# Kernel tuning notes

Hardware: AMD Instinct MI355X
Metric: run time of the kernel (lower is better)

## Reference

```python
import jax, jax.numpy as jnp
import numpy as np

NUM_HEADS = 4


def setup_inputs() -> dict:
    key = jax.random.key(0)
    k1, k2, k3 = jax.random.split(key, 3)
    B, NN, C = 1, 256, 128
    x = jax.random.normal(k1, (B, NN, C), dtype=jnp.float32)
    # Linear(d_model, 4*d_model, bias=False); stored as (in, out) for x @ W_w
    W_w = jax.random.normal(k2, (C, 4 * C), dtype=jnp.float32) * (C ** -0.5)
    # proj = Linear(d_model, d_model) with bias; stored as (in, out)
    W_proj = jax.random.normal(k3, (C, C), dtype=jnp.float32) * (C ** -0.5)
    b_proj = jnp.zeros((C,), dtype=jnp.float32)
    return {"x": x, "W_w": W_w, "W_proj": W_proj, "b_proj": b_proj}


def reference(x, W_w, W_proj, b_proj):
    B, NN, C = x.shape
    H = NUM_HEADS
    D = C // H
    scale = D ** -0.5
    # qkv-style projection: (B, NN, 4, H, D) -> (4, B, H, NN, D)
    w = (x @ W_w).reshape(B, NN, 4, H, D).transpose(2, 0, 3, 1, 4)
    a, b, c, v = w[0], w[1], w[2], w[3]
    AB = jnp.einsum('bhid,bhjd->bhij', a, b) * scale
    CD = jnp.einsum('bhid,bhkd->bhik', a, c) * scale
    EF = jnp.einsum('bhjd,bhkd->bhjk', b, c) * scale
    # Triplet scores: (B, H, NN, NN, NN)
    A_ijk = AB[..., :, :, None] + CD[..., :, None, :] + EF[..., None, :, :]
    e = jnp.exp(A_ijk)
    # Normalize over (i, j) for each k, per original sum(dim=(-2,-3))
    norm = jnp.clip(e.sum(axis=(-2, -3), keepdims=True), 1e-6, None)
    en = e / norm
    x1 = jnp.einsum('bhijk,bhjd->bhid', en, v)
    x2 = jnp.einsum('bhijk,bhkd->bhid', en, v)
    out = (x1 * x2).transpose(0, 2, 1, 3).reshape(B, NN, C)
    return out @ W_proj + b_proj
```

## Files before the change

kernel.cpp:

```cpp
#include <hip/hip_runtime.h>
#include <hip/hip_bf16.h>


constexpr size_t OFF_W     = 0;
constexpr size_t OFF_P     = 131072;
constexpr size_t OFF_Q     = OFF_P + 262144;
constexpr size_t OFF_RT    = OFF_Q + 262144;
constexpr size_t OFF_T     = OFF_RT + 262144;
constexpr size_t OFF_NORMP = OFF_T + 524288;

__global__ __launch_bounds__(256) void k_w(const float* __restrict__ x,
                                           const float* __restrict__ Ww,
                                           float* __restrict__ w,
                                           const float* __restrict__ bp,
                                           float* __restrict__ out) {
    __shared__ __align__(16) float As[1152];
    __shared__ __align__(16) float Bs[1152];
    int j0 = blockIdx.x * 32, i0 = blockIdx.y * 32;
    int t = threadIdx.x, tx = t & 15, ty = t >> 4, r = t >> 3, g = t & 7;
    {
        int oidx = (blockIdx.y * 16 + blockIdx.x) * 256 + t;
        out[oidx] = bp[oidx & 127];
    }
    float4 a4 = *(const float4*)&x[(size_t)(i0 + r) * 128 + g * 4];
    float4 b4 = *(const float4*)&Ww[(size_t)r * 512 + j0 + g * 4];
    float a00 = 0, a01 = 0, a10 = 0, a11 = 0;
    for (int kc = 0; kc < 128; kc += 32) {
        As[(g * 4 + 0) * 36 + r] = a4.x; As[(g * 4 + 1) * 36 + r] = a4.y;
        As[(g * 4 + 2) * 36 + r] = a4.z; As[(g * 4 + 3) * 36 + r] = a4.w;
        *(float4*)&Bs[r * 36 + g * 4] = b4;
        __syncthreads();
        if (kc + 32 < 128) {
            a4 = *(const float4*)&x[(size_t)(i0 + r) * 128 + kc + 32 + g * 4];
            b4 = *(const float4*)&Ww[(size_t)(kc + 32 + r) * 512 + j0 + g * 4];
        }
#pragma unroll
        for (int kk = 0; kk < 32; kk++) {
            float2 av = *(float2*)&As[kk * 36 + ty * 2];
            float2 bv = *(float2*)&Bs[kk * 36 + tx * 2];
            a00 += av.x * bv.x; a01 += av.x * bv.y;
            a10 += av.y * bv.x; a11 += av.y * bv.y;
        }
        __syncthreads();
    }
    *(float2*)&w[(size_t)(i0 + ty * 2) * 512 + j0 + tx * 2] = make_float2(a00, a01);
    *(float2*)&w[(size_t)(i0 + ty * 2 + 1) * 512 + j0 + tx * 2] = make_float2(a10, a11);
}

__global__ __launch_bounds__(256, 2) void k_T(const float* __restrict__ w,
                                              float* __restrict__ P,
                                              float* __restrict__ Q,
                                              float* __restrict__ Rt,
                                              float* __restrict__ T,
                                              float* __restrict__ normp) {
    __shared__ __align__(16) float aT[1152];
    __shared__ __align__(16) float cT[1152];
    __shared__ __align__(16) float bT[1152];
    __shared__ __align__(16) float PsT[1152];
    __shared__ __align__(16) float RsT[1152];
    int h = blockIdx.z >> 1, jh = blockIdx.z & 1;
    int k0 = blockIdx.x * 32, i0 = blockIdx.y * 32;
    int jc0 = jh * 128;
    size_t hb = (size_t)h * 65536;
    int t = threadIdx.x, tx = t & 15, ty = t >> 4, r = t >> 3, g = t & 7;
    const float sc = 0.17677669529663687f;

    float4 av = *(const float4*)&w[(size_t)(i0 + r) * 512 + h * 32 + g * 4];
    aT[(g * 4 + 0) * 36 + r] = av.x; aT[(g * 4 + 1) * 36 + r] = av.y;
    aT[(g * 4 + 2) * 36 + r] = av.z; aT[(g * 4 + 3) * 36 + r] = av.w;
    float4 cv = *(const float4*)&w[(size_t)(k0 + r) * 512 + 256 + h * 32 + g * 4];
    cT[(g * 4 + 0) * 36 + r] = cv.x; cT[(g * 4 + 1) * 36 + r] = cv.y;
    cT[(g * 4 + 2) * 36 + r] = cv.z; cT[(g * 4 + 3) * 36 + r] = cv.w;
    float4 bv = *(const float4*)&w[(size_t)(jc0 + r) * 512 + 128 + h * 32 + g * 4];
    __syncthreads();

    float2 a_tx[32], c_tx[32];
#pragma unroll
    for (int d = 0; d < 32; d++) {
        a_tx[d] = *(float2*)&aT[d * 36 + 2 * tx];
        c_tx[d] = *(float2*)&cT[d * 36 + 2 * tx];
    }

    float dq00 = 0, dq01 = 0, dq10 = 0, dq11 = 0;
#pragma unroll
    for (int d = 0; d < 32; d++) {
        float2 a2 = *(float2*)&aT[d * 36 + 2 * ty];
        float2 c2 = c_tx[d];
        dq00 += a2.x * c2.x; dq01 += a2.x * c2.y;
        dq10 += a2.y * c2.x; dq11 += a2.y * c2.y;
    }
    float q00 = __expf(sc * dq00), q01 = __expf(sc * dq01);
    float q10 = __expf(sc * dq10), q11 = __expf(sc * dq11);
    if (jh == 0) {
        *(float2*)&Q[hb + (size_t)(i0 + ty * 2) * 256 + k0 + tx * 2] = make_float2(q00, q01);
        *(float2*)&Q[hb + (size_t)(i0 + ty * 2 + 1) * 256 + k0 + tx * 2] = make_float2(q10, q11);
    }

    const bool wP = (k0 == 0), wR = (blockIdx.y == 0);
    float acc00 = 0, acc01 = 0, acc10 = 0, acc11 = 0;
    for (int jc = jc0; jc < jc0 + 128; jc += 32) {
        bT[(g * 4 + 0) * 36 + r] = bv.x; bT[(g * 4 + 1) * 36 + r] = bv.y;
        bT[(g * 4 + 2) * 36 + r] = bv.z; bT[(g * 4 + 3) * 36 + r] = bv.w;
        __syncthreads();
        if (jc + 32 < jc0 + 128)
            bv = *(const float4*)&w[(size_t)(jc + 32 + r) * 512 + 128 + h * 32 + g * 4];
        float dp00 = 0, dp01 = 0, dp10 = 0, dp11 = 0;
        float dr00 = 0, dr01 = 0, dr10 = 0, dr11 = 0;
#pragma unroll
        for (int d = 0; d < 32; d++) {
            float2 b2 = *(float2*)&bT[d * 36 + 2 * ty];
            float2 a2 = a_tx[d];
            float2 c2 = c_tx[d];
            dp00 += b2.x * a2.x; dp01 += b2.x * a2.y;
            dp10 += b2.y * a2.x; dp11 += b2.y * a2.y;
            dr00 += b2.x * c2.x; dr01 += b2.x * c2.y;
            dr10 += b2.y * c2.x; dr11 += b2.y * c2.y;
        }
        float p00 = __expf(sc * dp00), p01 = __expf(sc * dp01);
        float p10 = __expf(sc * dp10), p11 = __expf(sc * dp11);
        float r00 = __expf(sc * dr00), r01 = __expf(sc * dr01);
        float r10 = __expf(sc * dr10), r11 = __expf(sc * dr11);
        *(float2*)&PsT[(2 * tx + 0) * 36 + 2 * ty] = make_float2(p00, p10);
        *(float2*)&PsT[(2 * tx + 1) * 36 + 2 * ty] = make_float2(p01, p11);
        *(float2*)&RsT[(2 * tx + 0) * 36 + 2 * ty] = make_float2(r00, r10);
        *(float2*)&RsT[(2 * tx + 1) * 36 + 2 * ty] = make_float2(r01, r11);
        if (wP) {
            *(float2*)&P[hb + (size_t)(i0 + tx * 2 + 0) * 256 + jc + ty * 2] = make_float2(p00, p10);
            *(float2*)&P[hb + (size_t)(i0 + tx * 2 + 1) * 256 + jc + ty * 2] = make_float2(p01, p11);
        }
        if (wR) {
            *(float2*)&Rt[hb + (size_t)(k0 + tx * 2 + 0) * 256 + jc + ty * 2] = make_float2(r00, r10);
            *(float2*)&Rt[hb + (size_t)(k0 + tx * 2 + 1) * 256 + jc + ty * 2] = make_float2(r01, r11);
        }
        __syncthreads();
#pragma unroll
        for (int q = 0; q < 8; q++) {
            float4 pA = *(float4*)&PsT[(2 * ty + 0) * 36 + 4 * q];
            float4 pB = *(float4*)&PsT[(2 * ty + 1) * 36 + 4 * q];
            float4 rA = *(float4*)&RsT[(2 * tx + 0) * 36 + 4 * q];
            float4 rB = *(float4*)&RsT[(2 * tx + 1) * 36 + 4 * q];
            acc00 += pA.x * rA.x + pA.y * rA.y + pA.z * rA.z + pA.w * rA.w;
            acc01 += pA.x * rB.x + pA.y * rB.y + pA.z * rB.z + pA.w * rB.w;
            acc10 += pB.x * rA.x + pB.y * rA.y + pB.z * rA.z + pB.w * rA.w;
            acc11 += pB.x * rB.x + pB.y * rB.y + pB.z * rB.z + pB.w * rB.w;
        }
    }
    float* Tp = T + (size_t)jh * 262144;
    *(float2*)&Tp[hb + (size_t)(i0 + ty * 2) * 256 + k0 + tx * 2] = make_float2(acc00, acc01);
    *(float2*)&Tp[hb + (size_t)(i0 + ty * 2 + 1) * 256 + k0 + tx * 2] = make_float2(acc10, acc11);
    __syncthreads();
    float* red = PsT;
    red[ty * 34 + tx * 2]     = q00 * acc00 + q10 * acc10;
    red[ty * 34 + tx * 2 + 1] = q01 * acc01 + q11 * acc11;
    __syncthreads();
    if (t < 32) {
        float s = 0.f;
#pragma unroll
        for (int m = 0; m < 16; m++) s += red[m * 34 + t];
        normp[h * 4096 + (jh * 8 + blockIdx.y) * 256 + k0 + t] = s;
    }
}

__global__ __launch_bounds__(256) void k_x1x2S(
    const float* __restrict__ P, const float* __restrict__ Q,
    const float* __restrict__ Rt, const float* __restrict__ T,
    const float* __restrict__ normp, const float* __restrict__ w,
    const float* __restrict__ Wp, float* __restrict__ out) {
    int h = blockIdx.y;
    int i0 = blockIdx.x * 4;
    size_t hb = (size_t)h * 65536;
    __shared__ float rn_s[256];
    __shared__ __align__(16) float qs[1024];
    __shared__ __align__(16) float Ss[1024];
    __shared__ __align__(16) float wp[1024];
    __shared__ __align__(16) float wq[1024];
    __shared__ __align__(16) float vT[8320];
    __shared__ float ys[144];
    int t = threadIdx.x;
    {
        float s = 0.f;
#pragma unroll
        for (int ib = 0; ib < 16; ib++) s += normp[h * 4096 + ib * 256 + t];
        rn_s[t] = 1.f / fmaxf(s, 1e-6f);
    }
    __syncthreads();
    {
        int row = t >> 6, jq = (t & 63) * 4;
        float4 q4 = *(const float4*)&Q[hb + (size_t)(i0 + row) * 256 + jq];
        float4 rn4 = *(float4*)&rn_s[jq];
        q4.x *= rn4.x; q4.y *= rn4.y; q4.z *= rn4.z; q4.w *= rn4.w;
        *(float4*)&qs[row * 256 + jq] = q4;
    }
    __syncthreads();
    {
        int jq = (t & 63) * 4, kq = t >> 6;
        float4 acc0 = {0, 0, 0, 0}, acc1 = {0, 0, 0, 0};
        float4 acc2 = {0, 0, 0, 0}, acc3 = {0, 0, 0, 0};
#pragma unroll 8
        for (int kk = 0; kk < 64; kk++) {
            int k = kq * 64 + kk;
            float4 r4 = *(const float4*)&Rt[hb + (size_t)k * 256 + jq];
            float q0 = qs[0 * 256 + k], q1 = qs[1 * 256 + k];
            float q2 = qs[2 * 256 + k], q3 = qs[3 * 256 + k];
            acc0.x += q0 * r4.x; acc0.y += q0 * r4.y; acc0.z += q0 * r4.z; acc0.w += q0 * r4.w;
            acc1.x += q1 * r4.x; acc1.y += q1 * r4.y; acc1.z += q1 * r4.z; acc1.w += q1 * r4.w;
            acc2.x += q2 * r4.x; acc2.y += q2 * r4.y; acc2.z += q2 * r4.z; acc2.w += q2 * r4.w;
            acc3.x += q3 * r4.x; acc3.y += q3 * r4.y; acc3.z += q3 * r4.z; acc3.w += q3 * r4.w;
        }
        float* red = vT;
        *(float4*)&red[(kq * 4 + 0) * 256 + jq] = acc0;
        *(float4*)&red[(kq * 4 + 1) * 256 + jq] = acc1;
        *(float4*)&red[(kq * 4 + 2) * 256 + jq] = acc2;
        *(float4*)&red[(kq * 4 + 3) * 256 + jq] = acc3;
    }
    __syncthreads();
    {
        int row = t >> 6, jq = (t & 63) * 4;
        float* red = vT;
        float4 s0 = *(float4*)&red[(0 * 4 + row) * 256 + jq];
        float4 s1 = *(float4*)&red[(1 * 4 + row) * 256 + jq];
        float4 s2 = *(float4*)&red[(2 * 4 + row) * 256 + jq];
        float4 s3 = *(float4*)&red[(3 * 4 + row) * 256 + jq];
        float4 sm;
        sm.x = (s0.x + s1.x) + (s2.x + s3.x);
        sm.y = (s0.y + s1.y) + (s2.y + s3.y);
        sm.z = (s0.z + s1.z) + (s2.z + s3.z);
        sm.w = (s0.w + s1.w) + (s2.w + s3.w);
        *(float4*)&Ss[row * 256 + jq] = sm;
    }
    __syncthreads();
#pragma unroll
    for (int m = 0; m < 8; m++) {
        int jj = m * 32 + (t >> 3);
        int dd = (t & 7) * 4;
        float4 v4 = *(const float4*)&w[(size_t)jj * 512 + 384 + h * 32 + dd];
        vT[(dd + 0) * 260 + jj] = v4.x;
        vT[(dd + 1) * 260 + jj] = v4.y;
        vT[(dd + 2) * 260 + jj] = v4.z;
        vT[(dd + 3) * 260 + jj] = v4.w;
    }
    {
        int rr = t >> 6, jj = (t & 63) * 4;
        size_t o = hb + (size_t)(i0 + rr) * 256 + jj;
        float4 p4  = *(const float4*)&P[o];
        float4 t4a = *(const float4*)&T[o];
        float4 t4b = *(const float4*)&T[o + 262144];
        float4 q4  = *(float4*)&qs[rr * 256 + jj];
        float4 s4  = *(float4*)&Ss[rr * 256 + jj];
        float4 wpv, wqv;
        wpv.x = p4.x * s4.x; wpv.y = p4.y * s4.y;
        wpv.z = p4.z * s4.z; wpv.w = p4.w * s4.w;
        wqv.x = q4.x * (t4a.x + t4b.x); wqv.y = q4.y * (t4a.y + t4b.y);
        wqv.z = q4.z * (t4a.z + t4b.z); wqv.w = q4.w * (t4a.w + t4b.w);
        *(float4*)&wp[rr * 256 + jj] = wpv;
        *(float4*)&wq[rr * 256 + jj] = wqv;
    }
    __syncthreads();
    int d = t & 31, rl = (t >> 5) & 3, jh2 = t >> 7;
    int jbase = jh2 * 128;
    float x1 = 0.f, x2 = 0.f;
#pragma unroll
    for (int q = 0; q < 32; q++) {
        int j = jbase + 4 * q;
        float4 wp4 = *(float4*)&wp[rl * 256 + j];
        float4 wq4 = *(float4*)&wq[rl * 256 + j];
        float4 v4  = *(float4*)&vT[d * 260 + j];
        x1 += wp4.x * v4.x + wp4.y * v4.y + wp4.z * v4.z + wp4.w * v4.w;
        x2 += wq4.x * v4.x + wq4.y * v4.y + wq4.z * v4.z + wq4.w * v4.w;
    }
    __syncthreads();
    float* redx = wp;
    float* redy = wq;
    redx[t] = x1;
    redy[t] = x2;
    float* Wps = vT;
#pragma unroll
    for (int m = 0; m < 4; m++) {
        int idx = m * 256 + t;
        int k = idx >> 5, n = (idx & 31) * 4;
        *(float4*)&Wps[k * 128 + n] = *(const float4*)&Wp[(size_t)(h * 32 + k) * 128 + n];
    }
    __syncthreads();
    if (t < 128) {
        float x1t = redx[t] + redx[t + 128];
        float x2t = redy[t] + redy[t + 128];
        ys[rl * 33 + d] = x1t * x2t;
    }
    __syncthreads();
    int n = t & 127, ti = t >> 7;
    float acc0 = 0.f, acc1 = 0.f;
#pragma unroll
    for (int k = 0; k < 32; k++) {
        float wv = Wps[k * 128 + n];
        acc0 += ys[(ti + 0) * 33 + k] * wv;
        acc1 += ys[(ti + 2) * 33 + k] * wv;
    }
    atomicAdd(&out[(size_t)(i0 + ti + 0) * 128 + n], acc0);
    atomicAdd(&out[(size_t)(i0 + ti + 2) * 128 + n], acc1);
}

extern "C" void kernel_launch(void* const* d_in, const int* in_sizes, int n_in,
                              void* d_out, int out_size, void* d_ws, size_t ws_size,
                              hipStream_t stream) {
    const float* x      = (const float*)d_in[0];
    const float* W_w    = (const float*)d_in[1];
    const float* W_proj = (const float*)d_in[2];
    const float* b_proj = (const float*)d_in[3];
    float* out = (float*)d_out;
    float* ws  = (float*)d_ws;

    float* w     = ws + OFF_W;
    float* P     = ws + OFF_P;
    float* Q     = ws + OFF_Q;
    float* Rt    = ws + OFF_RT;
    float* T     = ws + OFF_T;
    float* normp = ws + OFF_NORMP;

    k_w<<<dim3(16, 8), 256, 0, stream>>>(x, W_w, w, b_proj, out);
    k_T<<<dim3(8, 8, 8), 256, 0, stream>>>(w, P, Q, Rt, T, normp);
    k_x1x2S<<<dim3(64, 4), 256, 0, stream>>>(P, Q, Rt, T, normp, w, W_proj, out);
}
```

Before: 36.52 us.

## Split k_T j-range into four partial slices and pad LDS stride to 38

The j reduction in k_T is now split four ways instead of two, doubling the grid to 1024 blocks, each covering 64 j columns. Four partial T buffers and twice as many normp partials are written, and the consumer kernel sums all of them. The shared-memory row stride also changes from 36 to 38 to alter bank mapping. This is meant to give more parallelism and shorten each block's serial loop, at the cost of redundant a/c/Q setup per block and extra partial-sum traffic.

Result: slower. 41.75 us (+14.3%).

```diff
diff --git a/kernel.cpp b/kernel.cpp
--- a/kernel.cpp
+++ b/kernel.cpp
@@ -7,7 +7,7 @@
 constexpr size_t OFF_Q     = OFF_P + 262144;
 constexpr size_t OFF_RT    = OFF_Q + 262144;
 constexpr size_t OFF_T     = OFF_RT + 262144;
-constexpr size_t OFF_NORMP = OFF_T + 524288;
+constexpr size_t OFF_NORMP = OFF_T + 1048576;
 
 __global__ __launch_bounds__(256) void k_w(const float* __restrict__ x,
                                            const float* __restrict__ Ww,
@@ -53,62 +53,62 @@
                                               float* __restrict__ Rt,
                                               float* __restrict__ T,
                                               float* __restrict__ normp) {
-    __shared__ __align__(16) float aT[1152];
-    __shared__ __align__(16) float cT[1152];
-    __shared__ __align__(16) float bT[1152];
-    __shared__ __align__(16) float PsT[1152];
-    __shared__ __align__(16) float RsT[1152];
-    int h = blockIdx.z >> 1, jh = blockIdx.z & 1;
+    __shared__ __align__(16) float aT[1216];
+    __shared__ __align__(16) float cT[1216];
+    __shared__ __align__(16) float bT[1216];
+    __shared__ __align__(16) float PsT[1216];
+    __shared__ __align__(16) float RsT[1216];
+    int h = blockIdx.z >> 2, jq = blockIdx.z & 3;
     int k0 = blockIdx.x * 32, i0 = blockIdx.y * 32;
-    int jc0 = jh * 128;
+    int jc0 = jq * 64;
     size_t hb = (size_t)h * 65536;
     int t = threadIdx.x, tx = t & 15, ty = t >> 4, r = t >> 3, g = t & 7;
     const float sc = 0.17677669529663687f;
 
     float4 av = *(const float4*)&w[(size_t)(i0 + r) * 512 + h * 32 + g * 4];
-    aT[(g * 4 + 0) * 36 + r] = av.x; aT[(g * 4 + 1) * 36 + r] = av.y;
-    aT[(g * 4 + 2) * 36 + r] = av.z; aT[(g * 4 + 3) * 36 + r] = av.w;
+    aT[(g * 4 + 0) * 38 + r] = av.x; aT[(g * 4 + 1) * 38 + r] = av.y;
+    aT[(g * 4 + 2) * 38 + r] = av.z; aT[(g * 4 + 3) * 38 + r] = av.w;
     float4 cv = *(const float4*)&w[(size_t)(k0 + r) * 512 + 256 + h * 32 + g * 4];
-    cT[(g * 4 + 0) * 36 + r] = cv.x; cT[(g * 4 + 1) * 36 + r] = cv.y;
-    cT[(g * 4 + 2) * 36 + r] = cv.z; cT[(g * 4 + 3) * 36 + r] = cv.w;
+    cT[(g * 4 + 0) * 38 + r] = cv.x; cT[(g * 4 + 1) * 38 + r] = cv.y;
+    cT[(g * 4 + 2) * 38 + r] = cv.z; cT[(g * 4 + 3) * 38 + r] = cv.w;
     float4 bv = *(const float4*)&w[(size_t)(jc0 + r) * 512 + 128 + h * 32 + g * 4];
     __syncthreads();
 
     float2 a_tx[32], c_tx[32];
 #pragma unroll
     for (int d = 0; d < 32; d++) {
-        a_tx[d] = *(float2*)&aT[d * 36 + 2 * tx];
-        c_tx[d] = *(float2*)&cT[d * 36 + 2 * tx];
+        a_tx[d] = *(float2*)&aT[d * 38 + 2 * tx];
+        c_tx[d] = *(float2*)&cT[d * 38 + 2 * tx];
     }
 
     float dq00 = 0, dq01 = 0, dq10 = 0, dq11 = 0;
 #pragma unroll
     for (int d = 0; d < 32; d++) {
-        float2 a2 = *(float2*)&aT[d * 36 + 2 * ty];
+        float2 a2 = *(float2*)&aT[d * 38 + 2 * ty];
         float2 c2 = c_tx[d];
         dq00 += a2.x * c2.x; dq01 += a2.x * c2.y;
         dq10 += a2.y * c2.x; dq11 += a2.y * c2.y;
     }
     float q00 = __expf(sc * dq00), q01 = __expf(sc * dq01);
     float q10 = __expf(sc * dq10), q11 = __expf(sc * dq11);
-    if (jh == 0) {
+    if (jq == 0) {
         *(float2*)&Q[hb + (size_t)(i0 + ty * 2) * 256 + k0 + tx * 2] = make_float2(q00, q01);
         *(float2*)&Q[hb + (size_t)(i0 + ty * 2 + 1) * 256 + k0 + tx * 2] = make_float2(q10, q11);
     }
 
     const bool wP = (k0 == 0), wR = (blockIdx.y == 0);
     float acc00 = 0, acc01 = 0, acc10 = 0, acc11 = 0;
-    for (int jc = jc0; jc < jc0 + 128; jc += 32) {
-        bT[(g * 4 + 0) * 36 + r] = bv.x; bT[(g * 4 + 1) * 36 + r] = bv.y;
-        bT[(g * 4 + 2) * 36 + r] = bv.z; bT[(g * 4 + 3) * 36 + r] = bv.w;
+    for (int jc = jc0; jc < jc0 + 64; jc += 32) {
+        bT[(g * 4 + 0) * 38 + r] = bv.x; bT[(g * 4 + 1) * 38 + r] = bv.y;
+        bT[(g * 4 + 2) * 38 + r] = bv.z; bT[(g * 4 + 3) * 38 + r] = bv.w;
         __syncthreads();
-        if (jc + 32 < jc0 + 128)
+        if (jc + 32 < jc0 + 64)
             bv = *(const float4*)&w[(size_t)(jc + 32 + r) * 512 + 128 + h * 32 + g * 4];
         float dp00 = 0, dp01 = 0, dp10 = 0, dp11 = 0;
         float dr00 = 0, dr01 = 0, dr10 = 0, dr11 = 0;
 #pragma unroll
         for (int d = 0; d < 32; d++) {
-            float2 b2 = *(float2*)&bT[d * 36 + 2 * ty];
+            float2 b2 = *(float2*)&bT[d * 38 + 2 * ty];
             float2 a2 = a_tx[d];
             float2 c2 = c_tx[d];
             dp00 += b2.x * a2.x; dp01 += b2.x * a2.y;
@@ -120,10 +120,10 @@
         float p10 = __expf(sc * dp10), p11 = __expf(sc * dp11);
         float r00 = __expf(sc * dr00), r01 = __expf(sc * dr01);
         float r10 = __expf(sc * dr10), r11 = __expf(sc * dr11);
-        *(float2*)&PsT[(2 * tx + 0) * 36 + 2 * ty] = make_float2(p00, p10);
-        *(float2*)&PsT[(2 * tx + 1) * 36 + 2 * ty] = make_float2(p01, p11);
-        *(float2*)&RsT[(2 * tx + 0) * 36 + 2 * ty] = make_float2(r00, r10);
-        *(float2*)&RsT[(2 * tx + 1) * 36 + 2 * ty] = make_float2(r01, r11);
+        *(float2*)&PsT[(2 * tx + 0) * 38 + 2 * ty] = make_float2(p00, p10);
+        *(float2*)&PsT[(2 * tx + 1) * 38 + 2 * ty] = make_float2(p01, p11);
+        *(float2*)&RsT[(2 * tx + 0) * 38 + 2 * ty] = make_float2(r00, r10);
+        *(float2*)&RsT[(2 * tx + 1) * 38 + 2 * ty] = make_float2(r01, r11);
         if (wP) {
             *(float2*)&P[hb + (size_t)(i0 + tx * 2 + 0) * 256 + jc + ty * 2] = make_float2(p00, p10);
             *(float2*)&P[hb + (size_t)(i0 + tx * 2 + 1) * 256 + jc + ty * 2] = make_float2(p01, p11);
@@ -135,17 +135,17 @@
         __syncthreads();
 #pragma unroll
         for (int q = 0; q < 8; q++) {
-            float4 pA = *(float4*)&PsT[(2 * ty + 0) * 36 + 4 * q];
-            float4 pB = *(float4*)&PsT[(2 * ty + 1) * 36 + 4 * q];
-            float4 rA = *(float4*)&RsT[(2 * tx + 0) * 36 + 4 * q];
-            float4 rB = *(float4*)&RsT[(2 * tx + 1) * 36 + 4 * q];
+            float4 pA = *(float4*)&PsT[(2 * ty + 0) * 38 + 4 * q];
+            float4 pB = *(float4*)&PsT[(2 * ty + 1) * 38 + 4 * q];
+            float4 rA = *(float4*)&RsT[(2 * tx + 0) * 38 + 4 * q];
+            float4 rB = *(float4*)&RsT[(2 * tx + 1) * 38 + 4 * q];
             acc00 += pA.x * rA.x + pA.y * rA.y + pA.z * rA.z + pA.w * rA.w;
             acc01 += pA.x * rB.x + pA.y * rB.y + pA.z * rB.z + pA.w * rB.w;
             acc10 += pB.x * rA.x + pB.y * rA.y + pB.z * rA.z + pB.w * rA.w;
             acc11 += pB.x * rB.x + pB.y * rB.y + pB.z * rB.z + pB.w * rB.w;
         }
     }
-    float* Tp = T + (size_t)jh * 262144;
+    float* Tp = T + (size_t)jq * 262144;
     *(float2*)&Tp[hb + (size_t)(i0 + ty * 2) * 256 + k0 + tx * 2] = make_float2(acc00, acc01);
     *(float2*)&Tp[hb + (size_t)(i0 + ty * 2 + 1) * 256 + k0 + tx * 2] = make_float2(acc10, acc11);
     __syncthreads();
@@ -157,7 +157,7 @@
         float s = 0.f;
 #pragma unroll
         for (int m = 0; m < 16; m++) s += red[m * 34 + t];
-        normp[h * 4096 + (jh * 8 + blockIdx.y) * 256 + k0 + t] = s;
+        normp[h * 8192 + (jq * 8 + blockIdx.y) * 256 + k0 + t] = s;
     }
 }
 
@@ -180,26 +180,26 @@
     {
         float s = 0.f;
 #pragma unroll
-        for (int ib = 0; ib < 16; ib++) s += normp[h * 4096 + ib * 256 + t];
+        for (int ib = 0; ib < 32; ib++) s += normp[h * 8192 + ib * 256 + t];
         rn_s[t] = 1.f / fmaxf(s, 1e-6f);
     }
     __syncthreads();
     {
-        int row = t >> 6, jq = (t & 63) * 4;
-        float4 q4 = *(const float4*)&Q[hb + (size_t)(i0 + row) * 256 + jq];
-        float4 rn4 = *(float4*)&rn_s[jq];
+        int row = t >> 6, jqc = (t & 63) * 4;
+        float4 q4 = *(const float4*)&Q[hb + (size_t)(i0 + row) * 256 + jqc];
+        float4 rn4 = *(float4*)&rn_s[jqc];
         q4.x *= rn4.x; q4.y *= rn4.y; q4.z *= rn4.z; q4.w *= rn4.w;
-        *(float4*)&qs[row * 256 + jq] = q4;
-    }
-    __syncthreads();
-    {
-        int jq = (t & 63) * 4, kq = t >> 6;
+        *(float4*)&qs[row * 256 + jqc] = q4;
+    }
+    __syncthreads();
+    {
+        int jqc = (t & 63) * 4, kq = t >> 6;
         float4 acc0 = {0, 0, 0, 0}, acc1 = {0, 0, 0, 0};
         float4 acc2 = {0, 0, 0, 0}, acc3 = {0, 0, 0, 0};
 #pragma unroll 8
         for (int kk = 0; kk < 64; kk++) {
             int k = kq * 64 + kk;
-            float4 r4 = *(const float4*)&Rt[hb + (size_t)k * 256 + jq];
+            float4 r4 = *(const float4*)&Rt[hb + (size_t)k * 256 + jqc];
             float q0 = qs[0 * 256 + k], q1 = qs[1 * 256 + k];
             float q2 = qs[2 * 256 + k], q3 = qs[3 * 256 + k];
             acc0.x += q0 * r4.x; acc0.y += q0 * r4.y; acc0.z += q0 * r4.z; acc0.w += q0 * r4.w;
@@ -208,25 +208,25 @@
             acc3.x += q3 * r4.x; acc3.y += q3 * r4.y; acc3.z += q3 * r4.z; acc3.w += q3 * r4.w;
         }
         float* red = vT;
-        *(float4*)&red[(kq * 4 + 0) * 256 + jq] = acc0;
-        *(float4*)&red[(kq * 4 + 1) * 256 + jq] = acc1;
-        *(float4*)&red[(kq * 4 + 2) * 256 + jq] = acc2;
-        *(float4*)&red[(kq * 4 + 3) * 256 + jq] = acc3;
-    }
-    __syncthreads();
-    {
-        int row = t >> 6, jq = (t & 63) * 4;
+        *(float4*)&red[(kq * 4 + 0) * 256 + jqc] = acc0;
+        *(float4*)&red[(kq * 4 + 1) * 256 + jqc] = acc1;
+        *(float4*)&red[(kq * 4 + 2) * 256 + jqc] = acc2;
+        *(float4*)&red[(kq * 4 + 3) * 256 + jqc] = acc3;
+    }
+    __syncthreads();
+    {
+        int row = t >> 6, jqc = (t & 63) * 4;
         float* red = vT;
-        float4 s0 = *(float4*)&red[(0 * 4 + row) * 256 + jq];
-        float4 s1 = *(float4*)&red[(1 * 4 + row) * 256 + jq];
-        float4 s2 = *(float4*)&red[(2 * 4 + row) * 256 + jq];
-        float4 s3 = *(float4*)&red[(3 * 4 + row) * 256 + jq];
+        float4 s0 = *(float4*)&red[(0 * 4 + row) * 256 + jqc];
+        float4 s1 = *(float4*)&red[(1 * 4 + row) * 256 + jqc];
+        float4 s2 = *(float4*)&red[(2 * 4 + row) * 256 + jqc];
+        float4 s3 = *(float4*)&red[(3 * 4 + row) * 256 + jqc];
         float4 sm;
         sm.x = (s0.x + s1.x) + (s2.x + s3.x);
         sm.y = (s0.y + s1.y) + (s2.y + s3.y);
         sm.z = (s0.z + s1.z) + (s2.z + s3.z);
         sm.w = (s0.w + s1.w) + (s2.w + s3.w);
-        *(float4*)&Ss[row * 256 + jq] = sm;
+        *(float4*)&Ss[row * 256 + jqc] = sm;
     }
     __syncthreads();
 #pragma unroll
@@ -245,13 +245,17 @@
         float4 p4  = *(const float4*)&P[o];
         float4 t4a = *(const float4*)&T[o];
         float4 t4b = *(const float4*)&T[o + 262144];
+        float4 t4c = *(const float4*)&T[o + 524288];
+        float4 t4d = *(const float4*)&T[o + 786432];
         float4 q4  = *(float4*)&qs[rr * 256 + jj];
         float4 s4  = *(float4*)&Ss[rr * 256 + jj];
         float4 wpv, wqv;
         wpv.x = p4.x * s4.x; wpv.y = p4.y * s4.y;
         wpv.z = p4.z * s4.z; wpv.w = p4.w * s4.w;
-        wqv.x = q4.x * (t4a.x + t4b.x); wqv.y = q4.y * (t4a.y + t4b.y);
-        wqv.z = q4.z * (t4a.z + t4b.z); wqv.w = q4.w * (t4a.w + t4b.w);
+        wqv.x = q4.x * ((t4a.x + t4b.x) + (t4c.x + t4d.x));
+        wqv.y = q4.y * ((t4a.y + t4b.y) + (t4c.y + t4d.y));
+        wqv.z = q4.z * ((t4a.z + t4b.z) + (t4c.z + t4d.z));
+        wqv.w = q4.w * ((t4a.w + t4b.w) + (t4c.w + t4d.w));
         *(float4*)&wp[rr * 256 + jj] = wpv;
         *(float4*)&wq[rr * 256 + jj] = wqv;
     }
@@ -317,6 +321,6 @@
     float* normp = ws + OFF_NORMP;
 
     k_w<<<dim3(16, 8), 256, 0, stream>>>(x, W_w, w, b_proj, out);
-    k_T<<<dim3(8, 8, 8), 256, 0, stream>>>(w, P, Q, Rt, T, normp);
+    k_T<<<dim3(8, 8, 16), 256, 0, stream>>>(w, P, Q, Rt, T, normp);
     k_x1x2S<<<dim3(64, 4), 256, 0, stream>>>(P, Q, Rt, T, normp, w, W_proj, out);
 }
```
